# Performance work log

Hardware: AMD Instinct MI355X
Metric: run time of the kernel (lower is better)

## Reference

```python
import jax, jax.numpy as jnp
import numpy as np

B, N_LAT, N_PAT = 32, 64, 4096
DIM_LAT = DIM_PAT = DIM_ATTN = 192
H = 6
HD = DIM_ATTN // H  # 32
SCALE = HD ** -0.5


def setup_inputs() -> dict:
    key = jax.random.key(0)
    ks = jax.random.split(key, 8)
    s = lambda fan_in: 1.0 / np.sqrt(fan_in)
    return {
        "x_latents": jax.random.normal(ks[0], (B, N_LAT, DIM_LAT), jnp.float32),
        "x_patches": jax.random.normal(ks[1], (B, N_PAT, DIM_PAT), jnp.float32),
        # weights stored [in, out] (torch Linear applies x @ W.T; math identical)
        "W_rv_lat": jax.random.uniform(ks[2], (DIM_LAT, 2 * DIM_ATTN), jnp.float32, -s(DIM_LAT), s(DIM_LAT)),
        "W_rv_pat": jax.random.uniform(ks[3], (DIM_PAT, 2 * DIM_ATTN), jnp.float32, -s(DIM_PAT), s(DIM_PAT)),
        "W_proj_lat": jax.random.uniform(ks[4], (DIM_ATTN, DIM_LAT), jnp.float32, -s(DIM_ATTN), s(DIM_ATTN)),
        "b_proj_lat": jax.random.uniform(ks[5], (DIM_LAT,), jnp.float32, -s(DIM_ATTN), s(DIM_ATTN)),
        "W_proj_pat": jax.random.uniform(ks[6], (DIM_ATTN, DIM_PAT), jnp.float32, -s(DIM_ATTN), s(DIM_ATTN)),
        "b_proj_pat": jax.random.uniform(ks[7], (DIM_PAT,), jnp.float32, -s(DIM_ATTN), s(DIM_ATTN)),
    }


def _split_rv(x, W, n):
    # x: [B, n, d_in] -> r, v each [B, H, n, HD]
    rv = (x @ W).reshape(x.shape[0], n, 2, H, HD)
    rv = jnp.transpose(rv, (2, 0, 3, 1, 4))  # [2, B, H, n, HD]
    return rv[0], rv[1]


def reference(x_latents, x_patches, W_rv_lat, W_rv_pat,
              W_proj_lat, b_proj_lat, W_proj_pat, b_proj_pat):
    r_lat, v_lat = _split_rv(x_latents, W_rv_lat, N_LAT)   # [B,H,N_lat,HD]
    r_pat, v_pat = _split_rv(x_patches, W_rv_pat, N_PAT)   # [B,H,N_pat,HD]

    # single score matrix, softmaxed along both axes (dropout = 0, eval mode)
    scores = jnp.einsum('bhld,bhpd->bhlp', r_lat, r_pat) * SCALE  # [B,H,N_lat,N_pat]
    attn = jax.nn.softmax(scores, axis=-1)    # row-wise (over patches)
    attn_T = jax.nn.softmax(scores, axis=-2)  # col-wise (over latents)

    out_lat = jnp.einsum('bhlp,bhpd->blhd', attn, v_pat).reshape(B, N_LAT, DIM_ATTN)
    out_pat = jnp.einsum('bhlp,bhld->bphd', attn_T, v_lat).reshape(B, N_PAT, DIM_ATTN)

    out_lat = out_lat @ W_proj_lat + b_proj_lat
    out_pat = out_pat @ W_proj_pat + b_proj_pat
    return out_lat, out_pat
```

## Files before the change

kernel.cpp:

```cpp
#include <hip/hip_runtime.h>

#define B_   32
#define NL_  64
#define NP_  4096
#define DIM_ 192
#define H_   6
#define HD_  32
#define PC_  128
#define NCH_ (NP_/PC_)
#define CPB_ 4
#define NSC_ (NCH_/CPB_)

typedef unsigned short u16;
typedef __attribute__((ext_vector_type(8))) short bf16x8;
typedef __attribute__((ext_vector_type(4))) short bf16x4;
typedef __attribute__((ext_vector_type(4))) float f32x4;

#define MFMA16(a,b,c) __builtin_amdgcn_mfma_f32_16x16x32_bf16(a,b,c,0,0,0)

__device__ __forceinline__ float bf2f(u16 s){ return __builtin_bit_cast(float,(unsigned)s<<16); }
__device__ __forceinline__ u16 f2bf(float f){
  unsigned u = __builtin_bit_cast(unsigned,f);
  return (u16)((u + 0x7FFFu + ((u>>16)&1u))>>16);
}

__global__ void k0_transpose(const float* __restrict__ W0, const float* __restrict__ W1,
                             const float* __restrict__ W2, const float* __restrict__ W3,
                             u16* __restrict__ T0, u16* __restrict__ T1,
                             u16* __restrict__ T2, u16* __restrict__ T3){
  int m = blockIdx.x >> 4, sub = blockIdx.x & 15;
  const float* src; u16* dst; int R, C;
  if      (m==0){src=W0;dst=T0;R=192;C=384;}
  else if (m==1){src=W1;dst=T1;R=192;C=384;}
  else if (m==2){src=W2;dst=T2;R=192;C=192;}
  else          {src=W3;dst=T3;R=192;C=192;}
  int total = R*C;
  for (int o = sub*256 + threadIdx.x; o < total; o += 16*256){
    int c = o / R, r = o - c*R;
    dst[o] = f2bf(src[r*C + c]);
  }
}

__global__ __launch_bounds__(512,2) void k_rv(const float* __restrict__ X,
    const u16* __restrict__ Wt, u16* __restrict__ R, u16* __restrict__ V,
    int Nseq, int nshift){
  __shared__ u16 Bs[96*200];
  const int t = threadIdx.x;
  const int m0 = blockIdx.x*256, nh = blockIdx.y;
  const int lane = t & 63, w = t >> 6, g = lane >> 4, ln = lane & 15;
  const f32x4 ZF = {0.f,0.f,0.f,0.f};
  u16* const dstA = nh ? V : R;

  bf16x8 af[2][6];
  #pragma unroll
  for (int i=0;i<2;i++)
    #pragma unroll
    for (int kk=0;kk<6;kk++){
      const float* s = &X[(size_t)(m0 + w*32 + i*16 + ln)*192 + kk*32 + g*8];
      float4 x0 = *(const float4*)s;
      float4 x1 = *(const float4*)(s+4);
      bf16x8 v;
      v[0]=(short)f2bf(x0.x); v[1]=(short)f2bf(x0.y); v[2]=(short)f2bf(x0.z); v[3]=(short)f2bf(x0.w);
      v[4]=(short)f2bf(x1.x); v[5]=(short)f2bf(x1.y); v[6]=(short)f2bf(x1.z); v[7]=(short)f2bf(x1.w);
      af[i][kk] = v;
    }

  size_t mbase[2];
  #pragma unroll
  for (int i=0;i<2;i++){
    int m = m0 + w*32 + i*16 + ln;
    int b = m >> nshift, sidx = m & (Nseq-1);
    mbase[i] = ((size_t)b*H_*(size_t)Nseq + (size_t)sidx) << 5;
  }
  const size_t hstride = (size_t)Nseq << 5;

  #pragma unroll
  for (int p = 0; p < 2; ++p){
    if (p) __syncthreads();
    for (int e = t*8; e < 96*192; e += 4096){
      int row = e / 192, col = e - row*192;
      *(bf16x8*)&Bs[row*200 + col] =
        *(const bf16x8*)&Wt[(size_t)(nh*192 + p*96 + row)*192 + col];
    }
    __syncthreads();

    f32x4 acc[6][2];
    #pragma unroll
    for(int j=0;j<6;j++){ acc[j][0]=ZF; acc[j][1]=ZF; }
    #pragma unroll
    for (int kk=0; kk<6; kk++)
      #pragma unroll
      for (int j=0; j<6; j++){
        bf16x8 bv = *(const bf16x8*)&Bs[(j*16 + ln)*200 + kk*32 + g*8];
        acc[j][0] = MFMA16(bv, af[0][kk], acc[j][0]);
        acc[j][1] = MFMA16(bv, af[1][kk], acc[j][1]);
      }
    #pragma unroll
    for(int j=0;j<6;j++){
      int c = p*96 + j*16 + g*4;
      int h = c >> 5, d0 = c & 31;
      #pragma unroll
      for(int i=0;i<2;i++){
        bf16x4 pk;
        #pragma unroll
        for(int r=0;r<4;r++) pk[r] = (short)f2bf(acc[j][i][r]);
        *(bf16x4*)&dstA[mbase[i] + (size_t)h*hstride + d0] = pk;
      }
    }
  }
}

__global__ __launch_bounds__(256) void k_attn(
    const u16* __restrict__ r_lat_g, const u16* __restrict__ v_lat_g,
    const u16* __restrict__ r_pat_g, const u16* __restrict__ v_pat_g,
    u16* __restrict__ Opat,
    float* __restrict__ numT_ws,
    float* __restrict__ rowsum_ws){
  const float SCALE = 0.17677669529663687f;
  const int sc = blockIdx.x, h = blockIdx.y, b = blockIdx.z;
  const int bh = b*H_ + h;
  const int t = threadIdx.x, lane = t&63, w = t>>6, g = lane>>4, ln = lane&15;
  __shared__ u16 RL [64*40];
  __shared__ u16 VLT[32*72];
  __shared__ u16 EN [128*72];
  __shared__ u16 ET [64*136];
  __shared__ float RS[4*64];
  __shared__ u16 POOL[128*40];
  u16* RP  = POOL;
  u16* VPT = POOL;
  const f32x4 ZF = {0.f,0.f,0.f,0.f};

  const size_t latbase = (size_t)bh * (NL_*HD_);
  { int row = t>>2, col = (t&3)*8;
    *(bf16x8*)&RL[row*40+col] = *(const bf16x8*)&r_lat_g[latbase + row*32 + col]; }
  { int l = t>>2, dd = (t&3)*8;
    bf16x8 v = *(const bf16x8*)&v_lat_g[latbase + l*32 + dd];
    #pragma unroll
    for(int jj=0;jj<8;jj++) VLT[(dd+jj)*72 + l] = (u16)v[jj]; }

  const int p0 = t>>2, dd0 = (t&3)*8;
  const size_t pb0 = ((size_t)bh*NP_ + (size_t)sc*(CPB_*PC_))*HD_;
  bf16x8 rcur0 = *(const bf16x8*)&r_pat_g[pb0 + (size_t)p0*32 + dd0];
  bf16x8 rcur1 = *(const bf16x8*)&r_pat_g[pb0 + (size_t)(64+p0)*32 + dd0];
  bf16x8 vcur0 = *(const bf16x8*)&v_pat_g[pb0 + (size_t)p0*32 + dd0];
  bf16x8 vcur1 = *(const bf16x8*)&v_pat_g[pb0 + (size_t)(64+p0)*32 + dd0];

  f32x4 nmT[2]; nmT[0]=ZF; nmT[1]=ZF;
  float rs[4] = {0.f,0.f,0.f,0.f};

  for (int c = 0; c < CPB_; ++c){
    *(bf16x8*)&RP[p0*40 + dd0]      = rcur0;
    *(bf16x8*)&RP[(64+p0)*40 + dd0] = rcur1;
    __syncthreads();

    f32x4 sf[2][4];
    { bf16x8 a0 = *(const bf16x8*)&RP[(w*32      + ln)*40 + g*8];
      bf16x8 a1 = *(const bf16x8*)&RP[(w*32 + 16 + ln)*40 + g*8];
      #pragma unroll
      for(int j=0;j<4;j++){
        bf16x8 bl = *(const bf16x8*)&RL[(j*16 + ln)*40 + g*8];
        sf[0][j] = MFMA16(a0, bl, ZF);
        sf[1][j] = MFMA16(a1, bl, ZF);
      } }

    bf16x8 rnxt0, rnxt1, vnxt0, vnxt1;
    const bool more = (c+1 < CPB_);
    if (more){
      const size_t pbn = pb0 + (size_t)(c+1)*(PC_*HD_);
      rnxt0 = *(const bf16x8*)&r_pat_g[pbn + (size_t)p0*32 + dd0];
      rnxt1 = *(const bf16x8*)&r_pat_g[pbn + (size_t)(64+p0)*32 + dd0];
      vnxt0 = *(const bf16x8*)&v_pat_g[pbn + (size_t)p0*32 + dd0];
      vnxt1 = *(const bf16x8*)&v_pat_g[pbn + (size_t)(64+p0)*32 + dd0];
    }

    float e[2][4][4], rcs[2][4];
    #pragma unroll
    for(int i=0;i<2;i++)
      #pragma unroll
      for(int r=0;r<4;r++){
        float cs = 0.f;
        #pragma unroll
        for(int j=0;j<4;j++){
          float ev = __expf(sf[i][j][r] * SCALE);
          e[i][j][r] = ev; cs += ev; rs[j] += ev;
        }
        cs += __shfl_xor(cs,1); cs += __shfl_xor(cs,2);
        cs += __shfl_xor(cs,4); cs += __shfl_xor(cs,8);
        rcs[i][r] = 1.0f / cs;
      }
    #pragma unroll
    for(int i=0;i<2;i++)
      #pragma unroll
      for(int j=0;j<4;j++){
        #pragma unroll
        for(int r=0;r<4;r++)
          EN[(w*32 + i*16 + g*4 + r)*72 + j*16 + ln] = f2bf(e[i][j][r]*rcs[i][r]);
        bf16x4 pk;
        #pragma unroll
        for(int r=0;r<4;r++) pk[r] = (short)f2bf(e[i][j][r]);
        *(bf16x4*)&ET[(j*16+ln)*136 + w*32 + i*16 + g*4] = pk;
      }
    __syncthreads();

    #pragma unroll
    for(int jj=0;jj<8;jj++){
      VPT[(dd0+jj)*136 + p0]      = (u16)vcur0[jj];
      VPT[(dd0+jj)*136 + 64 + p0] = (u16)vcur1[jj];
    }

    f32x4 opT[2][2];
    #pragma unroll
    for(int jd=0;jd<2;jd++){ opT[jd][0]=ZF; opT[jd][1]=ZF; }
    #pragma unroll
    for(int ks=0; ks<2; ks++){
      bf16x8 bv[2];
      #pragma unroll
      for(int jd=0;jd<2;jd++) bv[jd] = *(const bf16x8*)&VLT[(jd*16+ln)*72 + ks*32 + g*8];
      #pragma unroll
      for(int i=0;i<2;i++){
        bf16x8 afen = *(const bf16x8*)&EN[(w*32 + i*16 + ln)*72 + ks*32 + g*8];
        #pragma unroll
        for(int jd=0;jd<2;jd++) opT[jd][i] = MFMA16(bv[jd], afen, opT[jd][i]);
      }
    }
    const size_t obase = ((size_t)b*NP_ + (size_t)(sc*CPB_ + c)*PC_)*DIM_ + h*32;
    #pragma unroll
    for(int jd=0;jd<2;jd++)
      #pragma unroll
      for(int i=0;i<2;i++){
        int p = w*32 + i*16 + ln, d0 = jd*16 + g*4;
        bf16x4 pk;
        #pragma unroll
        for(int r=0;r<4;r++) pk[r] = (short)f2bf(opT[jd][i][r]);
        *(bf16x4*)&Opat[obase + (size_t)p*DIM_ + d0] = pk;
      }
    __syncthreads();

    #pragma unroll
    for(int ks=0; ks<4; ks++){
      bf16x8 afet = *(const bf16x8*)&ET[(w*16+ln)*136 + ks*32 + g*8];
      #pragma unroll
      for(int dj=0;dj<2;dj++){
        bf16x8 bv = *(const bf16x8*)&VPT[(dj*16+ln)*136 + ks*32 + g*8];
        nmT[dj] = MFMA16(bv, afet, nmT[dj]);
      }
    }
    __syncthreads();

    if (more){ rcur0=rnxt0; rcur1=rnxt1; vcur0=vnxt0; vcur1=vnxt1; }
  }

  #pragma unroll
  for(int j=0;j<4;j++){
    float vs = rs[j];
    vs += __shfl_xor(vs,16); vs += __shfl_xor(vs,32);
    if (g == 0) RS[w*64 + j*16 + ln] = vs;
  }
  __syncthreads();
  if (t < 64)
    rowsum_ws[((size_t)bh*NSC_ + sc)*64 + t] = RS[t] + RS[64+t] + RS[128+t] + RS[192+t];
  float* dstN = numT_ws + ((size_t)bh*NSC_ + sc)*2048;
  #pragma unroll
  for(int dj=0;dj<2;dj++){
    int l = w*16 + ln, d0 = dj*16 + g*4;
    *(f32x4*)&dstN[l*32 + d0] = nmT[dj];
  }
}

__global__ __launch_bounds__(256) void k_lat_reduce(const float* __restrict__ numT_ws,
    const float* __restrict__ rowsum_ws, u16* __restrict__ attn_lat){
  int bh = blockIdx.x, b = bh / H_, h = bh - b*H_;
  __shared__ float RSs[64];
  int t = threadIdx.x;
  if (t < 64){
    float s = 0.f;
    for(int c=0;c<NSC_;c++) s += rowsum_ws[((size_t)bh*NSC_ + c)*64 + t];
    RSs[t] = 1.0f / s;
  }
  __syncthreads();
  for(int idx = t; idx < 2048; idx += 256){
    int l = idx >> 5, dd = idx & 31;
    float s = 0.f;
    for(int c=0;c<NSC_;c++) s += numT_ws[((size_t)bh*NSC_ + c)*2048 + idx];
    attn_lat[((size_t)b*NL_ + l)*DIM_ + h*32 + dd] = f2bf(s * RSs[l]);
  }
}

__global__ __launch_bounds__(256) void k_proj_lat(const u16* __restrict__ A,
    const u16* __restrict__ Wt, const float* __restrict__ bias, float* __restrict__ out){
  int b = blockIdx.x;
  __shared__ u16 As[64*40];
  __shared__ u16 Bs[192*40];
  int t = threadIdx.x, lane = t&63, w = t>>6, g = lane>>4, ln = lane&15;
  const f32x4 ZF = {0.f,0.f,0.f,0.f};
  f32x4 acc[4][3];
  #pragma unroll
  for(int i=0;i<4;i++)
    #pragma unroll
    for(int j=0;j<3;j++) acc[i][j]=ZF;
  for(int k0=0;k0<192;k0+=32){
    bf16x8 av; bf16x8 bv[3];
    { int row = t>>2, col=(t&3)*8;
      av = *(const bf16x8*)&A[((size_t)b*NL_ + row)*DIM_ + k0 + col]; }
    #pragma unroll
    for(int it=0;it<3;it++){
      int e = it*2048 + t*8, row = e>>5, col = (t&3)*8;
      bv[it] = *(const bf16x8*)&Wt[(size_t)row*192 + k0 + col];
    }
    if (k0) __syncthreads();
    { int row = t>>2, col=(t&3)*8; *(bf16x8*)&As[row*40+col] = av; }
    #pragma unroll
    for(int it=0;it<3;it++){
      int e = it*2048 + t*8, row = e>>5, col = (t&3)*8;
      *(bf16x8*)&Bs[row*40+col] = bv[it];
    }
    __syncthreads();
    bf16x8 bw[3];
    #pragma unroll
    for(int jf=0;jf<3;jf++) bw[jf] = *(const bf16x8*)&Bs[(w*48 + jf*16 + ln)*40 + g*8];
    #pragma unroll
    for(int lf=0;lf<4;lf++){
      bf16x8 af = *(const bf16x8*)&As[(lf*16 + ln)*40 + g*8];
      #pragma unroll
      for(int jf=0;jf<3;jf++) acc[lf][jf] = MFMA16(af, bw[jf], acc[lf][jf]);
    }
  }
  #pragma unroll
  for(int lf=0;lf<4;lf++)
    #pragma unroll
    for(int jf=0;jf<3;jf++){
      int j = w*48 + jf*16 + ln;
      float bs = bias[j];
      #pragma unroll
      for(int r=0;r<4;r++){
        int l = lf*16 + g*4 + r;
        out[((size_t)b*NL_ + l)*DIM_ + j] = acc[lf][jf][r] + bs;
      }
    }
}

__global__ __launch_bounds__(512,2) void k_proj_pat(const u16* __restrict__ X,
    const u16* __restrict__ Wt, const float* __restrict__ bias, float* __restrict__ out){
  __shared__ u16 Bs[96*200];
  const int t = threadIdx.x;
  const int m0 = blockIdx.x*256;
  const int lane = t & 63, w = t >> 6, g = lane >> 4, ln = lane & 15;
  const f32x4 ZF = {0.f,0.f,0.f,0.f};

  bf16x8 af[2][6];
  #pragma unroll
  for (int i=0;i<2;i++)
    #pragma unroll
    for (int kk=0;kk<6;kk++)
      af[i][kk] = *(const bf16x8*)&X[(size_t)(m0 + w*32 + i*16 + ln)*192 + kk*32 + g*8];

  const int mrow0 = m0 + w*32 + ln, mrow1 = mrow0 + 16;

  #pragma unroll
  for (int p = 0; p < 2; ++p){
    if (p) __syncthreads();
    for (int e = t*8; e < 96*192; e += 4096){
      int row = e / 192, col = e - row*192;
      *(bf16x8*)&Bs[row*200 + col] =
        *(const bf16x8*)&Wt[(size_t)(p*96 + row)*192 + col];
    }
    __syncthreads();

    f32x4 acc[6][2];
    #pragma unroll
    for(int j=0;j<6;j++){ acc[j][0]=ZF; acc[j][1]=ZF; }
    #pragma unroll
    for (int kk=0; kk<6; kk++)
      #pragma unroll
      for (int j=0; j<6; j++){
        bf16x8 bv = *(const bf16x8*)&Bs[(j*16 + ln)*200 + kk*32 + g*8];
        acc[j][0] = MFMA16(bv, af[0][kk], acc[j][0]);
        acc[j][1] = MFMA16(bv, af[1][kk], acc[j][1]);
      }
    #pragma unroll
    for(int j=0;j<6;j++){
      int c = p*96 + j*16 + g*4;
      float4 bs4 = *(const float4*)&bias[c];
      float4 o0, o1;
      o0.x = acc[j][0][0] + bs4.x; o0.y = acc[j][0][1] + bs4.y;
      o0.z = acc[j][0][2] + bs4.z; o0.w = acc[j][0][3] + bs4.w;
      o1.x = acc[j][1][0] + bs4.x; o1.y = acc[j][1][1] + bs4.y;
      o1.z = acc[j][1][2] + bs4.z; o1.w = acc[j][1][3] + bs4.w;
      *(float4*)&out[(size_t)mrow0*192 + c] = o0;
      *(float4*)&out[(size_t)mrow1*192 + c] = o1;
    }
  }
}

extern "C" void kernel_launch(void* const* d_in, const int* in_sizes, int n_in,
                              void* d_out, int out_size, void* d_ws, size_t ws_size,
                              hipStream_t stream){
  const float* x_lat  = (const float*)d_in[0];
  const float* x_pat  = (const float*)d_in[1];
  const float* W_rv_l = (const float*)d_in[2];
  const float* W_rv_p = (const float*)d_in[3];
  const float* W_pj_l = (const float*)d_in[4];
  const float* b_pj_l = (const float*)d_in[5];
  const float* W_pj_p = (const float*)d_in[6];
  const float* b_pj_p = (const float*)d_in[7];
  float* out = (float*)d_out;

  char* ws = (char*)d_ws;
  size_t off = 0;
  auto alloc = [&](size_t bytes)->void*{ void* p = ws + off; off += (bytes + 255) & ~(size_t)255; return p; };
  u16* WtRL   = (u16*)alloc((size_t)384*192*2);
  u16* WtRP   = (u16*)alloc((size_t)384*192*2);
  u16* WtPL   = (u16*)alloc((size_t)192*192*2);
  u16* WtPP   = (u16*)alloc((size_t)192*192*2);
  u16* r_lat  = (u16*)alloc((size_t)B_*H_*NL_*HD_*2);
  u16* v_lat  = (u16*)alloc((size_t)B_*H_*NL_*HD_*2);
  u16* r_pat  = (u16*)alloc((size_t)B_*H_*NP_*HD_*2);
  u16* v_pat  = (u16*)alloc((size_t)B_*H_*NP_*HD_*2);
  u16* Opat   = (u16*)alloc((size_t)B_*NP_*DIM_*2);
  float* numT = (float*)alloc((size_t)B_*H_*NSC_*64*32*4);
  float* rsum = (float*)alloc((size_t)B_*H_*NSC_*64*4);
  u16* attn_l = (u16*)alloc((size_t)B_*NL_*DIM_*2);

  k0_transpose<<<64,256,0,stream>>>(W_rv_l, W_rv_p, W_pj_l, W_pj_p, WtRL, WtRP, WtPL, WtPP);
  k_rv<<<dim3((B_*NP_)/256, 2),512,0,stream>>>(x_pat, WtRP, r_pat, v_pat, NP_, 12);
  k_rv<<<dim3((B_*NL_)/256, 2),512,0,stream>>>(x_lat, WtRL, r_lat, v_lat, NL_, 6);
  k_attn<<<dim3(NSC_, H_, B_),256,0,stream>>>(r_lat, v_lat, r_pat, v_pat, Opat, numT, rsum);
  k_lat_reduce<<<B_*H_,256,0,stream>>>(numT, rsum, attn_l);
  k_proj_lat<<<B_,256,0,stream>>>(attn_l, WtPL, b_pj_l, out);
  k_proj_pat<<<dim3((B_*NP_)/256),512,0,stream>>>(Opat, WtPP, b_pj_p, out + (size_t)B_*NL_*DIM_);
}
```

Measured before the change: 202.0 us.

## Retile rv and patch-projection GEMMs to 64-row blocks, reorder VPT staging

Result: faster. 172.5 us (-14.6%).

```diff
diff --git a/kernel.cpp b/kernel.cpp
--- a/kernel.cpp
+++ b/kernel.cpp
@@ -41,71 +41,61 @@
   }
 }
 
-__global__ __launch_bounds__(512,2) void k_rv(const float* __restrict__ X,
+__global__ __launch_bounds__(256,8) void k_rv(const float* __restrict__ X,
     const u16* __restrict__ Wt, u16* __restrict__ R, u16* __restrict__ V,
     int Nseq, int nshift){
-  __shared__ u16 Bs[96*200];
+  __shared__ u16 Bs[64*200];
   const int t = threadIdx.x;
-  const int m0 = blockIdx.x*256, nh = blockIdx.y;
+  const int m0 = blockIdx.x*64;
   const int lane = t & 63, w = t >> 6, g = lane >> 4, ln = lane & 15;
+  const int srB = t >> 2, bq = t & 3;
   const f32x4 ZF = {0.f,0.f,0.f,0.f};
-  u16* const dstA = nh ? V : R;
-
-  bf16x8 af[2][6];
-  #pragma unroll
-  for (int i=0;i<2;i++)
-    #pragma unroll
-    for (int kk=0;kk<6;kk++){
-      const float* s = &X[(size_t)(m0 + w*32 + i*16 + ln)*192 + kk*32 + g*8];
-      float4 x0 = *(const float4*)s;
-      float4 x1 = *(const float4*)(s+4);
-      bf16x8 v;
-      v[0]=(short)f2bf(x0.x); v[1]=(short)f2bf(x0.y); v[2]=(short)f2bf(x0.z); v[3]=(short)f2bf(x0.w);
-      v[4]=(short)f2bf(x1.x); v[5]=(short)f2bf(x1.y); v[6]=(short)f2bf(x1.z); v[7]=(short)f2bf(x1.w);
-      af[i][kk] = v;
-    }
-
-  size_t mbase[2];
-  #pragma unroll
-  for (int i=0;i<2;i++){
-    int m = m0 + w*32 + i*16 + ln;
-    int b = m >> nshift, sidx = m & (Nseq-1);
-    mbase[i] = ((size_t)b*H_*(size_t)Nseq + (size_t)sidx) << 5;
-  }
+
+  bf16x8 af[6];
+  #pragma unroll
+  for (int kk=0;kk<6;kk++){
+    const float* s = &X[(size_t)(m0 + w*16 + ln)*192 + kk*32 + g*8];
+    float4 x0 = *(const float4*)s;
+    float4 x1 = *(const float4*)(s+4);
+    bf16x8 v;
+    v[0]=(short)f2bf(x0.x); v[1]=(short)f2bf(x0.y); v[2]=(short)f2bf(x0.z); v[3]=(short)f2bf(x0.w);
+    v[4]=(short)f2bf(x1.x); v[5]=(short)f2bf(x1.y); v[6]=(short)f2bf(x1.z); v[7]=(short)f2bf(x1.w);
+    af[kk] = v;
+  }
+
+  const int mrow = m0 + w*16 + ln;
+  const int b = mrow >> nshift, sidx = mrow & (Nseq-1);
+  const size_t mbase = ((size_t)b*H_*(size_t)Nseq + (size_t)sidx) << 5;
   const size_t hstride = (size_t)Nseq << 5;
 
-  #pragma unroll
-  for (int p = 0; p < 2; ++p){
-    if (p) __syncthreads();
-    for (int e = t*8; e < 96*192; e += 4096){
-      int row = e / 192, col = e - row*192;
-      *(bf16x8*)&Bs[row*200 + col] =
-        *(const bf16x8*)&Wt[(size_t)(nh*192 + p*96 + row)*192 + col];
-    }
-    __syncthreads();
-
-    f32x4 acc[6][2];
-    #pragma unroll
-    for(int j=0;j<6;j++){ acc[j][0]=ZF; acc[j][1]=ZF; }
+  for (int c = 0; c < 6; ++c){
+    if (c) __syncthreads();
+    #pragma unroll
+    for (int it=0; it<6; it++)
+      *(bf16x8*)&Bs[srB*200 + bq*48 + it*8] =
+        *(const bf16x8*)&Wt[(size_t)(c*64 + srB)*192 + bq*48 + it*8];
+    __syncthreads();
+
+    f32x4 acc[4];
+    #pragma unroll
+    for(int j=0;j<4;j++) acc[j]=ZF;
     #pragma unroll
     for (int kk=0; kk<6; kk++)
       #pragma unroll
-      for (int j=0; j<6; j++){
+      for (int j=0; j<4; j++){
         bf16x8 bv = *(const bf16x8*)&Bs[(j*16 + ln)*200 + kk*32 + g*8];
-        acc[j][0] = MFMA16(bv, af[0][kk], acc[j][0]);
-        acc[j][1] = MFMA16(bv, af[1][kk], acc[j][1]);
-      }
-    #pragma unroll
-    for(int j=0;j<6;j++){
-      int c = p*96 + j*16 + g*4;
-      int h = c >> 5, d0 = c & 31;
-      #pragma unroll
-      for(int i=0;i<2;i++){
-        bf16x4 pk;
-        #pragma unroll
-        for(int r=0;r<4;r++) pk[r] = (short)f2bf(acc[j][i][r]);
-        *(bf16x4*)&dstA[mbase[i] + (size_t)h*hstride + d0] = pk;
-      }
+        acc[j] = MFMA16(bv, af[kk], acc[j]);
+      }
+    #pragma unroll
+    for(int j=0;j<4;j++){
+      int nb = c*64 + j*16 + g*4;
+      u16* dst; int cc;
+      if (nb < 192){ dst = R; cc = nb; } else { dst = V; cc = nb - 192; }
+      int h = cc >> 5, d0 = cc & 31;
+      bf16x4 pk;
+      #pragma unroll
+      for(int r=0;r<4;r++) pk[r] = (short)f2bf(acc[j][r]);
+      *(bf16x4*)&dst[mbase + (size_t)h*hstride + d0] = pk;
     }
   }
 }
@@ -200,13 +190,6 @@
         for(int r=0;r<4;r++) pk[r] = (short)f2bf(e[i][j][r]);
         *(bf16x4*)&ET[(j*16+ln)*136 + w*32 + i*16 + g*4] = pk;
       }
-    __syncthreads();
-
-    #pragma unroll
-    for(int jj=0;jj<8;jj++){
-      VPT[(dd0+jj)*136 + p0]      = (u16)vcur0[jj];
-      VPT[(dd0+jj)*136 + 64 + p0] = (u16)vcur1[jj];
-    }
 
     f32x4 opT[2][2];
     #pragma unroll
@@ -234,6 +217,13 @@
         for(int r=0;r<4;r++) pk[r] = (short)f2bf(opT[jd][i][r]);
         *(bf16x4*)&Opat[obase + (size_t)p*DIM_ + d0] = pk;
       }
+    __syncthreads();
+
+    #pragma unroll
+    for(int jj=0;jj<8;jj++){
+      VPT[(dd0+jj)*136 + p0]      = (u16)vcur0[jj];
+      VPT[(dd0+jj)*136 + 64 + p0] = (u16)vcur1[jj];
+    }
     __syncthreads();
 
     #pragma unroll
@@ -339,55 +329,50 @@
     }
 }
 
-__global__ __launch_bounds__(512,2) void k_proj_pat(const u16* __restrict__ X,
+__global__ __launch_bounds__(256,8) void k_proj_pat(const u16* __restrict__ X,
     const u16* __restrict__ Wt, const float* __restrict__ bias, float* __restrict__ out){
-  __shared__ u16 Bs[96*200];
+  __shared__ u16 Bs[64*200];
   const int t = threadIdx.x;
-  const int m0 = blockIdx.x*256;
+  const int m0 = blockIdx.x*64;
   const int lane = t & 63, w = t >> 6, g = lane >> 4, ln = lane & 15;
+  const int srB = t >> 2, bq = t & 3;
   const f32x4 ZF = {0.f,0.f,0.f,0.f};
 
-  bf16x8 af[2][6];
-  #pragma unroll
-  for (int i=0;i<2;i++)
-    #pragma unroll
-    for (int kk=0;kk<6;kk++)
-      af[i][kk] = *(const bf16x8*)&X[(size_t)(m0 + w*32 + i*16 + ln)*192 + kk*32 + g*8];
-
-  const int mrow0 = m0 + w*32 + ln, mrow1 = mrow0 + 16;
-
-  #pragma unroll
-  for (int p = 0; p < 2; ++p){
-    if (p) __syncthreads();
-    for (int e = t*8; e < 96*192; e += 4096){
-      int row = e / 192, col = e - row*192;
-      *(bf16x8*)&Bs[row*200 + col] =
-        *(const bf16x8*)&Wt[(size_t)(p*96 + row)*192 + col];
-    }
-    __syncthreads();
-
-    f32x4 acc[6][2];
-    #pragma unroll
-    for(int j=0;j<6;j++){ acc[j][0]=ZF; acc[j][1]=ZF; }
+  bf16x8 af[6];
+  #pragma unroll
+  for (int kk=0;kk<6;kk++)
+    af[kk] = *(const bf16x8*)&X[(size_t)(m0 + w*16 + ln)*192 + kk*32 + g*8];
+
+  const int mrow = m0 + w*16 + ln;
+
+  for (int c = 0; c < 3; ++c){
+    if (c) __syncthreads();
+    #pragma unroll
+    for (int it=0; it<6; it++)
+      *(bf16x8*)&Bs[srB*200 + bq*48 + it*8] =
+        *(const bf16x8*)&Wt[(size_t)(c*64 + srB)*192 + bq*48 + it*8];
+    __syncthreads();
+
+    f32x4 acc[4];
+    #pragma unroll
+    for(int j=0;j<4;j++) acc[j]=ZF;
     #pragma unroll
     for (int kk=0; kk<6; kk++)
       #pragma unroll
-      for (int j=0; j<6; j++){
+      for (int j=0; j<4; j++){
         bf16x8 bv = *(const bf16x8*)&Bs[(j*16 + ln)*200 + kk*32 + g*8];
-        acc[j][0] = MFMA16(bv, af[0][kk], acc[j][0]);
-        acc[j][1] = MFMA16(bv, af[1][kk], acc[j][1]);
-      }
-    #pragma unroll
-    for(int j=0;j<6;j++){
-      int c = p*96 + j*16 + g*4;
-      float4 bs4 = *(const float4*)&bias[c];
-      float4 o0, o1;
-      o0.x = acc[j][0][0] + bs4.x; o0.y = acc[j][0][1] + bs4.y;
-      o0.z = acc[j][0][2] + bs4.z; o0.w = acc[j][0][3] + bs4.w;
-      o1.x = acc[j][1][0] + bs4.x; o1.y = acc[j][1][1] + bs4.y;
-      o1.z = acc[j][1][2] + bs4.z; o1.w = acc[j][1][3] + bs4.w;
-      *(float4*)&out[(size_t)mrow0*192 + c] = o0;
-      *(float4*)&out[(size_t)mrow1*192 + c] = o1;
+        acc[j] = MFMA16(bv, af[kk], acc[j]);
+      }
+    #pragma unroll
+    for(int j=0;j<4;j++){
+      int nb = c*64 + j*16 + g*4;
+      float4 bs4 = *(const float4*)&bias[nb];
+      float4 o;
+      o.x = acc[j][0] + bs4.x;
+      o.y = acc[j][1] + bs4.y;
+      o.z = acc[j][2] + bs4.z;
+      o.w = acc[j][3] + bs4.w;
+      *(float4*)&out[(size_t)mrow*192 + nb] = o;
     }
   }
 }
@@ -422,10 +407,10 @@
   u16* attn_l = (u16*)alloc((size_t)B_*NL_*DIM_*2);
 
   k0_transpose<<<64,256,0,stream>>>(W_rv_l, W_rv_p, W_pj_l, W_pj_p, WtRL, WtRP, WtPL, WtPP);
-  k_rv<<<dim3((B_*NP_)/256, 2),512,0,stream>>>(x_pat, WtRP, r_pat, v_pat, NP_, 12);
-  k_rv<<<dim3((B_*NL_)/256, 2),512,0,stream>>>(x_lat, WtRL, r_lat, v_lat, NL_, 6);
+  k_rv<<<dim3((B_*NP_)/64),256,0,stream>>>(x_pat, WtRP, r_pat, v_pat, NP_, 12);
+  k_rv<<<dim3((B_*NL_)/64),256,0,stream>>>(x_lat, WtRL, r_lat, v_lat, NL_, 6);
   k_attn<<<dim3(NSC_, H_, B_),256,0,stream>>>(r_lat, v_lat, r_pat, v_pat, Opat, numT, rsum);
   k_lat_reduce<<<B_*H_,256,0,stream>>>(numT, rsum, attn_l);
   k_proj_lat<<<B_,256,0,stream>>>(attn_l, WtPL, b_pj_l, out);
-  k_proj_pat<<<dim3((B_*NP_)/256),512,0,stream>>>(Opat, WtPP, b_pj_p, out + (size_t)B_*NL_*DIM_);
-}
+  k_proj_pat<<<dim3((B_*NP_)/64),256,0,stream>>>(Opat, WtPP, b_pj_p, out + (size_t)B_*NL_*DIM_);
+}
```
